# Performance work log

Measured on AMD Instinct MI355X. Metric: run time of the kernel, lower is better.

## Reference

```python
import jax, jax.numpy as jnp
import numpy as np

B, D, H, L = 131072, 128, 128, 4
LN_EPS = 1e-5


def _layernorm(x, gamma, beta):
    mu = jnp.mean(x, axis=-1, keepdims=True)
    var = jnp.mean(jnp.square(x - mu), axis=-1, keepdims=True)
    return (x - mu) * jax.lax.rsqrt(var + LN_EPS) * gamma + beta


def setup_inputs() -> dict:
    key = jax.random.key(0)
    ks = jax.random.split(key, 12)
    t = jax.random.uniform(ks[0], (1,), dtype=jnp.float32)
    p = jax.random.normal(ks[1], (B, D), dtype=jnp.float32)
    w = jax.random.normal(ks[2], (B, D), dtype=jnp.float32)
    # VectorField parameters (torch default inits approximated with scaled normals)
    W_in = jax.random.normal(ks[3], (H, D), dtype=jnp.float32) * (1.0 / np.sqrt(D))
    b_in = jax.random.normal(ks[4], (H,), dtype=jnp.float32) * 0.01
    # FourierFeature buffers, scale=1.0 (hard-coded in VectorField)
    fw = jax.random.normal(ks[5], (L, H), dtype=jnp.float32) * 1.0
    fb = jax.random.uniform(ks[6], (L, H), dtype=jnp.float32) * 1.0
    gamma = jnp.ones((L, H), dtype=jnp.float32)
    beta = jnp.zeros((L, H), dtype=jnp.float32)
    Wl = jax.random.normal(ks[7], (L, H, H), dtype=jnp.float32) * (1.0 / np.sqrt(H))
    bl = jax.random.normal(ks[8], (L, H), dtype=jnp.float32) * 0.01
    W_out = jax.random.normal(ks[9], (D, H), dtype=jnp.float32) * (1.0 / np.sqrt(H))
    b_out = jax.random.normal(ks[10], (D,), dtype=jnp.float32) * 0.01
    return {"t": t, "p": p, "w": w, "W_in": W_in, "b_in": b_in, "fw": fw,
            "fb": fb, "gamma": gamma, "beta": beta, "Wl": Wl, "bl": bl,
            "W_out": W_out, "b_out": b_out}


def reference(t, p, w, W_in, b_in, fw, fb, gamma, beta, Wl, bl, W_out, b_out):
    # VectorField.forward: all ops act per-row, so batched vjp == vmapped per-sample vjp
    def vf(pp):  # pp: [B, D]
        h = pp @ W_in.T + b_in                      # [B, H]
        for i in range(L):
            h = h + jnp.sin(t * fw[i] + fb[i])      # time embedding, broadcast [H]
            h = jax.nn.softplus(h)
            h = _layernorm(h, gamma[i], beta[i])
            h = h @ Wl[i].T + bl[i]
        return h @ W_out.T + b_out                  # [B, D]

    dp, vjp_fn = jax.vjp(vf, p)
    dw = -vjp_fn(w)[0]
    return dp, dw
```

## Files before the change

kernel.cpp:

```cpp
#include <hip/hip_runtime.h>

typedef unsigned short u16;
typedef unsigned int   u32;
typedef __attribute__((ext_vector_type(8))) short bf16x8;
typedef __attribute__((ext_vector_type(4))) float f32x4;

#define NB 131072
#define LN_EPS 1e-5f
#define EX_STRIDE 136

__device__ __forceinline__ u16 f2b(float f){
  union { __bf16 h; u16 u; } c; c.h = (__bf16)f; return c.u;
}
__device__ __forceinline__ float upk(u32 pr, int hi){
  union { u32 u; float f; } c; c.u = hi ? (pr & 0xFFFF0000u) : (pr << 16); return c.f;
}
__device__ __forceinline__ float rowsum16(float x){
  x += __shfl_xor(x, 1);
  x += __shfl_xor(x, 2);
  x += __shfl_xor(x, 4);
  x += __shfl_xor(x, 8);
  return x;
}
__device__ __forceinline__ bf16x8 cvt8(const float* __restrict__ s){
  f32x4 x0 = *(const f32x4*)s;
  f32x4 x1 = *(const f32x4*)(s + 4);
  bf16x8 r;
  r[0]=(short)f2b(x0[0]); r[1]=(short)f2b(x0[1]);
  r[2]=(short)f2b(x0[2]); r[3]=(short)f2b(x0[3]);
  r[4]=(short)f2b(x1[0]); r[5]=(short)f2b(x1[1]);
  r[6]=(short)f2b(x1[2]); r[7]=(short)f2b(x1[3]);
  return r;
}

__device__ __forceinline__ void glds16(const u16* g, u16* l){
  __builtin_amdgcn_global_load_lds(
      (const __attribute__((address_space(1))) void*)g,
      (__attribute__((address_space(3))) void*)l, 16, 0, 0);
}
__device__ __forceinline__ void stageB(const u16* __restrict__ packB, int m,
                                       u16* __restrict__ bst, int wave, int lane){
  const u16* src = packB + m*16384 + wave*512 + lane*8;
  u16*       dst = bst   + wave*512;
  #pragma unroll
  for (int k = 0; k < 8; k++)
    glds16(src + k*2048, dst + k*2048);
}

__device__ __forceinline__ void gemm16(const bf16x8 a[4], const u16* __restrict__ Blds,
                                       int lane, f32x4 C[8]){
  const bf16x8* Bf = (const bf16x8*)Blds;
  #pragma unroll
  for (int nt = 0; nt < 8; nt++){
    f32x4 c = {0.f, 0.f, 0.f, 0.f};
    #pragma unroll
    for (int kt = 0; kt < 4; kt++){
      bf16x8 b = Bf[(nt*4 + kt)*64 + lane];
      c = __builtin_amdgcn_mfma_f32_16x16x32_bf16(a[kt], b, c, 0, 0, 0);
    }
    C[nt] = c;
  }
}

__global__ void prep_kernel(const float* __restrict__ t,   const float* __restrict__ W_in,
                            const float* __restrict__ b_in,const float* __restrict__ fw,
                            const float* __restrict__ fb,  const float* __restrict__ gamma,
                            const float* __restrict__ beta,const float* __restrict__ Wl,
                            const float* __restrict__ bl,  const float* __restrict__ W_out,
                            const float* __restrict__ b_out,
                            u16* __restrict__ packB, float* __restrict__ vecs)
{
  int bid = blockIdx.x, tid = threadIdx.x;
  if (bid < 768){
    int e    = bid*256 + tid;
    int m    = e >> 14;
    int r    = e & 16383;
    int fi   = r >> 9;
    int lane = (r >> 3) & 63;
    int j    = r & 7;
    int nt = fi >> 2, kt = fi & 3;
    int k = kt*32 + (lane >> 4)*8 + j;
    int n = nt*16 + (lane & 15);
    const float* src; bool tr;
    if      (m == 0){ src = W_in;              tr = true;  }
    else if (m <= 4){ src = Wl + (m-1)*16384;  tr = true;  }
    else if (m == 5){ src = W_out;             tr = true;  }
    else if (m == 6){ src = W_out;             tr = false; }
    else if (m <=10){ src = Wl + (m-7)*16384;  tr = false; }
    else            { src = W_in;              tr = false; }
    float v = tr ? src[n*128 + k] : src[k*128 + n];
    if      (m >= 1 && m <= 4)  v *= gamma[(m-1)*128 + k];
    else if (m >= 7 && m <= 10) v *= gamma[(m-7)*128 + n];
    packB[e] = f2b(v);
  } else if (bid < 770){
    int idx = (bid - 768)*256 + tid;
    vecs[idx] = sinf(t[0] * fw[idx] + fb[idx]);
  } else if (bid < 772){
    int gid = (bid - 770)*256 + tid;
    int i = gid >> 7, o = gid & 127;
    const float* Wr = Wl + i*16384 + o*128;
    const float* be = beta + i*128;
    float acc = bl[gid];
    for (int k2 = 0; k2 < 128; k2++) acc += be[k2] * Wr[k2];
    vecs[512 + gid] = acc;
  } else {
    if (tid < 128) vecs[1024 + tid]        = b_in[tid];
    else           vecs[1152 + (tid-128)]  = b_out[tid-128];
  }
}

__global__ __launch_bounds__(256, 2)
void fused_vf(const float* __restrict__ p, const float* __restrict__ w,
              const u16* __restrict__ packB, const float* __restrict__ vecs,
              float* __restrict__ dp_out, float* __restrict__ dw_out)
{
  __shared__ __align__(16) u16  exch[4 * 16 * EX_STRIDE];
  __shared__ __align__(16) u16  bstage[16384];
  __shared__ float sv[1024];

  const int tid  = threadIdx.x;
  const int wave = tid >> 6, lane = tid & 63;
  const int l15  = lane & 15, quad = lane >> 4;
  u16* ex = exch + wave * 16 * EX_STRIDE;

  stageB(packB, 0, bstage, wave, lane);
  for (int idx = tid; idx < 1024; idx += 256) sv[idx] = vecs[idx];
  const float* sS   = sv;
  const float* sBl  = sv + 512;
  const float* gBin  = vecs + 1024;
  const float* gBout = vecs + 1152;

  const long rowBase = (long)blockIdx.x * 64 + wave * 16;

  u32   sp_ck[4][8][2];
  float mus[4][4];
  float invs[4][4];

  bf16x8 a[4];
  f32x4  C[8];

  {
    const float* pr = p + (size_t)(rowBase + l15)*128 + quad*8;
    #pragma unroll
    for (int kt = 0; kt < 4; kt++) a[kt] = cvt8(pr + kt*32);
  }
  __syncthreads();
  gemm16(a, bstage, lane, C);
  #pragma unroll
  for (int nt = 0; nt < 8; nt++){
    float bv = gBin[nt*16 + l15];
    #pragma unroll
    for (int r = 0; r < 4; r++) C[nt][r] += bv;
  }

  #pragma unroll
  for (int i = 0; i < 4; i++){
    __syncthreads();
    stageB(packB, 1+i, bstage, wave, lane);
    float sum[4] = {0,0,0,0}, ssq[4] = {0,0,0,0};
    #pragma unroll
    for (int nt = 0; nt < 8; nt++){
      float se = sS[i*128 + nt*16 + l15];
      #pragma unroll
      for (int r = 0; r < 4; r++){
        float x  = C[nt][r] + se;
        float e  = __expf(-fabsf(x));
        float li = __logf(1.0f + e);
        float sp = fmaxf(x, 0.0f) + li;
        u16 sb = f2b(sp);
        if (r & 1) sp_ck[i][nt][r>>1] |= ((u32)sb) << 16; else sp_ck[i][nt][r>>1] = sb;
        sum[r] += sp; ssq[r] += sp*sp;
        C[nt][r] = sp;
      }
    }
    float mu[4], inv[4];
    #pragma unroll
    for (int r = 0; r < 4; r++){
      float m1 = rowsum16(sum[r]) * (1.0f/128.0f);
      float m2 = rowsum16(ssq[r]) * (1.0f/128.0f);
      float var = m2 - m1*m1;
      mu[r] = m1; inv[r] = rsqrtf(fmaxf(var, 0.0f) + LN_EPS);
      mus[i][r] = m1; invs[i][r] = inv[r];
    }
    #pragma unroll
    for (int nt = 0; nt < 8; nt++)
      #pragma unroll
      for (int r = 0; r < 4; r++){
        float xh = (C[nt][r] - mu[r]) * inv[r];
        ex[(quad*4 + r)*EX_STRIDE + nt*16 + l15] = f2b(xh);
      }
    __syncthreads();
    {
      const u16* rp = ex + l15*EX_STRIDE + quad*8;
      #pragma unroll
      for (int kt = 0; kt < 4; kt++) a[kt] = *(const bf16x8*)(rp + kt*32);
    }
    gemm16(a, bstage, lane, C);
    #pragma unroll
    for (int nt = 0; nt < 8; nt++){
      float bv = sBl[i*128 + nt*16 + l15];
      #pragma unroll
      for (int r = 0; r < 4; r++) C[nt][r] += bv;
    }
  }

  __syncthreads();
  stageB(packB, 5, bstage, wave, lane);
  #pragma unroll
  for (int nt = 0; nt < 8; nt++)
    #pragma unroll
    for (int r = 0; r < 4; r++)
      ex[(quad*4 + r)*EX_STRIDE + nt*16 + l15] = f2b(C[nt][r]);
  __syncthreads();
  {
    const u16* rp = ex + l15*EX_STRIDE + quad*8;
    #pragma unroll
    for (int kt = 0; kt < 4; kt++) a[kt] = *(const bf16x8*)(rp + kt*32);
  }
  gemm16(a, bstage, lane, C);
  {
    float* gp = dp_out + (size_t)rowBase*128;
    #pragma unroll
    for (int nt = 0; nt < 8; nt++){
      float bv = gBout[nt*16 + l15];
      #pragma unroll
      for (int r = 0; r < 4; r++)
        gp[(size_t)(quad*4 + r)*128 + nt*16 + l15] = C[nt][r] + bv;
    }
  }

  __syncthreads();
  stageB(packB, 6, bstage, wave, lane);
  {
    const float* wr = w + (size_t)(rowBase + l15)*128 + quad*8;
    #pragma unroll
    for (int kt = 0; kt < 4; kt++) a[kt] = cvt8(wr + kt*32);
  }
  __syncthreads();
  gemm16(a, bstage, lane, C);
  __syncthreads();
  stageB(packB, 10, bstage, wave, lane);

  #pragma unroll
  for (int ii = 0; ii < 4; ii++){
    const int i = 3 - ii;
    #pragma unroll
    for (int nt = 0; nt < 8; nt++)
      #pragma unroll
      for (int r = 0; r < 4; r++)
        ex[(quad*4 + r)*EX_STRIDE + nt*16 + l15] = f2b(C[nt][r]);
    __syncthreads();
    {
      const u16* rp = ex + l15*EX_STRIDE + quad*8;
      #pragma unroll
      for (int kt = 0; kt < 4; kt++) a[kt] = *(const bf16x8*)(rp + kt*32);
    }
    gemm16(a, bstage, lane, C);
    __syncthreads();
    stageB(packB, (ii < 3) ? (7 + (2 - ii)) : 11, bstage, wave, lane);
    float s1[4] = {0,0,0,0}, s2[4] = {0,0,0,0};
    #pragma unroll
    for (int nt = 0; nt < 8; nt++)
      #pragma unroll
      for (int r = 0; r < 4; r++){
        float sp = upk(sp_ck[i][nt][r>>1], r & 1);
        float xh = (sp - mus[i][r]) * invs[i][r];
        float gx = C[nt][r];
        s1[r] += gx; s2[r] += gx * xh;
        C[nt][r] = gx;
      }
    float m1[4], m2[4];
    #pragma unroll
    for (int r = 0; r < 4; r++){
      m1[r] = rowsum16(s1[r]) * (1.0f/128.0f);
      m2[r] = rowsum16(s2[r]) * (1.0f/128.0f);
    }
    #pragma unroll
    for (int nt = 0; nt < 8; nt++)
      #pragma unroll
      for (int r = 0; r < 4; r++){
        float sp = upk(sp_ck[i][nt][r>>1], r & 1);
        float xh = (sp - mus[i][r]) * invs[i][r];
        float sg = 1.0f - __expf(-sp);
        float gu = invs[i][r] * (C[nt][r] - m1[r] - xh * m2[r]);
        C[nt][r] = gu * sg;
      }
  }

  #pragma unroll
  for (int nt = 0; nt < 8; nt++)
    #pragma unroll
    for (int r = 0; r < 4; r++)
      ex[(quad*4 + r)*EX_STRIDE + nt*16 + l15] = f2b(C[nt][r]);
  __syncthreads();
  {
    const u16* rp = ex + l15*EX_STRIDE + quad*8;
    #pragma unroll
    for (int kt = 0; kt < 4; kt++) a[kt] = *(const bf16x8*)(rp + kt*32);
  }
  gemm16(a, bstage, lane, C);
  {
    float* gp = dw_out + (size_t)rowBase*128;
    #pragma unroll
    for (int nt = 0; nt < 8; nt++)
      #pragma unroll
      for (int r = 0; r < 4; r++)
        gp[(size_t)(quad*4 + r)*128 + nt*16 + l15] = -C[nt][r];
  }
}

extern "C" void kernel_launch(void* const* d_in, const int* in_sizes, int n_in,
                              void* d_out, int out_size, void* d_ws, size_t ws_size,
                              hipStream_t stream)
{
  const float* t     = (const float*)d_in[0];
  const float* p     = (const float*)d_in[1];
  const float* w     = (const float*)d_in[2];
  const float* W_in  = (const float*)d_in[3];
  const float* b_in  = (const float*)d_in[4];
  const float* fw    = (const float*)d_in[5];
  const float* fb    = (const float*)d_in[6];
  const float* gamma = (const float*)d_in[7];
  const float* beta  = (const float*)d_in[8];
  const float* Wl    = (const float*)d_in[9];
  const float* bl    = (const float*)d_in[10];
  const float* W_out = (const float*)d_in[11];
  const float* b_out = (const float*)d_in[12];

  u16*   packB = (u16*)d_ws;
  float* vecs  = (float*)((char*)d_ws + 12*16384*2);

  prep_kernel<<<773, 256, 0, stream>>>(t, W_in, b_in, fw, fb, gamma, beta,
                                       Wl, bl, W_out, b_out, packB, vecs);

  float* dp = (float*)d_out;
  float* dw = (float*)d_out + (size_t)NB * 128;
  fused_vf<<<NB/64, 256, 0, stream>>>(p, w, packB, vecs, dp, dw);
}
```

Baseline: 386.0 us.

## Swap MFMA operands so each lane holds one row's features

The MFMA operands are swapped so weights are the A operand and activations the B operand, which transposes the accumulator layout: each lane now holds four consecutive features of a single row. Row reductions for LayerNorm shrink from four 4-step shuffle trees per row set to one 2-step shuffle across quads. LDS exchange writes become packed 8-byte stores, and the global output stores and bias loads become 16-byte vector accesses. This relies on the packed weight layout being valid under the swapped operand roles. It also reduces the per-lane mean and inverse-std state, which may lower register pressure.

After: 356.3 us. 7.7% less time.

```diff
diff --git a/kernel.cpp b/kernel.cpp
--- a/kernel.cpp
+++ b/kernel.cpp
@@ -4,6 +4,7 @@
 typedef unsigned int   u32;
 typedef __attribute__((ext_vector_type(8))) short bf16x8;
 typedef __attribute__((ext_vector_type(4))) float f32x4;
+typedef __attribute__((ext_vector_type(2))) unsigned int u32x2;
 
 #define NB 131072
 #define LN_EPS 1e-5f
@@ -12,14 +13,15 @@
 __device__ __forceinline__ u16 f2b(float f){
   union { __bf16 h; u16 u; } c; c.h = (__bf16)f; return c.u;
 }
+__device__ __forceinline__ u32 pk2(float a, float b){
+  return (u32)f2b(a) | ((u32)f2b(b) << 16);
+}
 __device__ __forceinline__ float upk(u32 pr, int hi){
   union { u32 u; float f; } c; c.u = hi ? (pr & 0xFFFF0000u) : (pr << 16); return c.f;
 }
-__device__ __forceinline__ float rowsum16(float x){
-  x += __shfl_xor(x, 1);
-  x += __shfl_xor(x, 2);
-  x += __shfl_xor(x, 4);
-  x += __shfl_xor(x, 8);
+__device__ __forceinline__ float qsum(float x){
+  x += __shfl_xor(x, 16);
+  x += __shfl_xor(x, 32);
   return x;
 }
 __device__ __forceinline__ bf16x8 cvt8(const float* __restrict__ s){
@@ -47,18 +49,18 @@
     glds16(src + k*2048, dst + k*2048);
 }
 
-__device__ __forceinline__ void gemm16(const bf16x8 a[4], const u16* __restrict__ Blds,
-                                       int lane, f32x4 C[8]){
-  const bf16x8* Bf = (const bf16x8*)Blds;
-  #pragma unroll
-  for (int nt = 0; nt < 8; nt++){
+__device__ __forceinline__ void gemm16s(const bf16x8 x[4], const u16* __restrict__ Blds,
+                                        int lane, f32x4 C[8]){
+  const bf16x8* Wf = (const bf16x8*)Blds;
+  #pragma unroll
+  for (int mt = 0; mt < 8; mt++){
     f32x4 c = {0.f, 0.f, 0.f, 0.f};
     #pragma unroll
     for (int kt = 0; kt < 4; kt++){
-      bf16x8 b = Bf[(nt*4 + kt)*64 + lane];
-      c = __builtin_amdgcn_mfma_f32_16x16x32_bf16(a[kt], b, c, 0, 0, 0);
-    }
-    C[nt] = c;
+      bf16x8 wfrag = Wf[(mt*4 + kt)*64 + lane];
+      c = __builtin_amdgcn_mfma_f32_16x16x32_bf16(wfrag, x[kt], c, 0, 0, 0);
+    }
+    C[mt] = c;
   }
 }
 
@@ -116,116 +118,100 @@
 {
   __shared__ __align__(16) u16  exch[4 * 16 * EX_STRIDE];
   __shared__ __align__(16) u16  bstage[16384];
-  __shared__ float sv[1024];
+  __shared__ __align__(16) float sv[1024];
 
   const int tid  = threadIdx.x;
   const int wave = tid >> 6, lane = tid & 63;
   const int l15  = lane & 15, quad = lane >> 4;
   u16* ex = exch + wave * 16 * EX_STRIDE;
+  u16*       exw = ex + l15*EX_STRIDE + quad*4;
+  const u16* exr = ex + l15*EX_STRIDE + quad*8;
 
   stageB(packB, 0, bstage, wave, lane);
   for (int idx = tid; idx < 1024; idx += 256) sv[idx] = vecs[idx];
-  const float* sS   = sv;
-  const float* sBl  = sv + 512;
+  const float* sS    = sv;
+  const float* sBl   = sv + 512;
   const float* gBin  = vecs + 1024;
   const float* gBout = vecs + 1152;
 
   const long rowBase = (long)blockIdx.x * 64 + wave * 16;
 
   u32   sp_ck[4][8][2];
-  float mus[4][4];
-  float invs[4][4];
-
-  bf16x8 a[4];
+  float mus[4];
+  float invs[4];
+
+  bf16x8 x[4];
   f32x4  C[8];
 
   {
     const float* pr = p + (size_t)(rowBase + l15)*128 + quad*8;
     #pragma unroll
-    for (int kt = 0; kt < 4; kt++) a[kt] = cvt8(pr + kt*32);
-  }
-  __syncthreads();
-  gemm16(a, bstage, lane, C);
-  #pragma unroll
-  for (int nt = 0; nt < 8; nt++){
-    float bv = gBin[nt*16 + l15];
-    #pragma unroll
-    for (int r = 0; r < 4; r++) C[nt][r] += bv;
-  }
+    for (int kt = 0; kt < 4; kt++) x[kt] = cvt8(pr + kt*32);
+  }
+  __syncthreads();
+  gemm16s(x, bstage, lane, C);
+  #pragma unroll
+  for (int mt = 0; mt < 8; mt++)
+    C[mt] += *(const f32x4*)(gBin + mt*16 + quad*4);
 
   #pragma unroll
   for (int i = 0; i < 4; i++){
     __syncthreads();
     stageB(packB, 1+i, bstage, wave, lane);
-    float sum[4] = {0,0,0,0}, ssq[4] = {0,0,0,0};
-    #pragma unroll
-    for (int nt = 0; nt < 8; nt++){
-      float se = sS[i*128 + nt*16 + l15];
+    float sum = 0.f, ssq = 0.f;
+    #pragma unroll
+    for (int mt = 0; mt < 8; mt++){
+      f32x4 se = *(const f32x4*)(sS + i*128 + mt*16 + quad*4);
       #pragma unroll
       for (int r = 0; r < 4; r++){
-        float x  = C[nt][r] + se;
-        float e  = __expf(-fabsf(x));
-        float li = __logf(1.0f + e);
-        float sp = fmaxf(x, 0.0f) + li;
+        float a_ = C[mt][r] + se[r];
+        float e  = __expf(-fabsf(a_));
+        float sp = fmaxf(a_, 0.0f) + __logf(1.0f + e);
         u16 sb = f2b(sp);
-        if (r & 1) sp_ck[i][nt][r>>1] |= ((u32)sb) << 16; else sp_ck[i][nt][r>>1] = sb;
-        sum[r] += sp; ssq[r] += sp*sp;
-        C[nt][r] = sp;
+        if (r & 1) sp_ck[i][mt][r>>1] |= ((u32)sb) << 16; else sp_ck[i][mt][r>>1] = sb;
+        sum += sp; ssq += sp*sp;
+        C[mt][r] = sp;
       }
     }
-    float mu[4], inv[4];
-    #pragma unroll
-    for (int r = 0; r < 4; r++){
-      float m1 = rowsum16(sum[r]) * (1.0f/128.0f);
-      float m2 = rowsum16(ssq[r]) * (1.0f/128.0f);
-      float var = m2 - m1*m1;
-      mu[r] = m1; inv[r] = rsqrtf(fmaxf(var, 0.0f) + LN_EPS);
-      mus[i][r] = m1; invs[i][r] = inv[r];
-    }
-    #pragma unroll
-    for (int nt = 0; nt < 8; nt++)
-      #pragma unroll
-      for (int r = 0; r < 4; r++){
-        float xh = (C[nt][r] - mu[r]) * inv[r];
-        ex[(quad*4 + r)*EX_STRIDE + nt*16 + l15] = f2b(xh);
-      }
+    float m1 = qsum(sum) * (1.0f/128.0f);
+    float m2 = qsum(ssq) * (1.0f/128.0f);
+    float inv = rsqrtf(fmaxf(m2 - m1*m1, 0.0f) + LN_EPS);
+    mus[i] = m1; invs[i] = inv;
+    #pragma unroll
+    for (int mt = 0; mt < 8; mt++){
+      u32x2 v;
+      v[0] = pk2((C[mt][0]-m1)*inv, (C[mt][1]-m1)*inv);
+      v[1] = pk2((C[mt][2]-m1)*inv, (C[mt][3]-m1)*inv);
+      *(u32x2*)(exw + mt*16) = v;
+    }
     __syncthreads();
-    {
-      const u16* rp = ex + l15*EX_STRIDE + quad*8;
-      #pragma unroll
-      for (int kt = 0; kt < 4; kt++) a[kt] = *(const bf16x8*)(rp + kt*32);
-    }
-    gemm16(a, bstage, lane, C);
-    #pragma unroll
-    for (int nt = 0; nt < 8; nt++){
-      float bv = sBl[i*128 + nt*16 + l15];
-      #pragma unroll
-      for (int r = 0; r < 4; r++) C[nt][r] += bv;
-    }
+    #pragma unroll
+    for (int kt = 0; kt < 4; kt++) x[kt] = *(const bf16x8*)(exr + kt*32);
+    gemm16s(x, bstage, lane, C);
+    #pragma unroll
+    for (int mt = 0; mt < 8; mt++)
+      C[mt] += *(const f32x4*)(sBl + i*128 + mt*16 + quad*4);
   }
 
   __syncthreads();
   stageB(packB, 5, bstage, wave, lane);
   #pragma unroll
-  for (int nt = 0; nt < 8; nt++)
-    #pragma unroll
-    for (int r = 0; r < 4; r++)
-      ex[(quad*4 + r)*EX_STRIDE + nt*16 + l15] = f2b(C[nt][r]);
-  __syncthreads();
+  for (int mt = 0; mt < 8; mt++){
+    u32x2 v;
+    v[0] = pk2(C[mt][0], C[mt][1]);
+    v[1] = pk2(C[mt][2], C[mt][3]);
+    *(u32x2*)(exw + mt*16) = v;
+  }
+  __syncthreads();
+  #pragma unroll
+  for (int kt = 0; kt < 4; kt++) x[kt] = *(const bf16x8*)(exr + kt*32);
+  gemm16s(x, bstage, lane, C);
   {
-    const u16* rp = ex + l15*EX_STRIDE + quad*8;
-    #pragma unroll
-    for (int kt = 0; kt < 4; kt++) a[kt] = *(const bf16x8*)(rp + kt*32);
-  }
-  gemm16(a, bstage, lane, C);
-  {
-    float* gp = dp_out + (size_t)rowBase*128;
-    #pragma unroll
-    for (int nt = 0; nt < 8; nt++){
-      float bv = gBout[nt*16 + l15];
-      #pragma unroll
-      for (int r = 0; r < 4; r++)
-        gp[(size_t)(quad*4 + r)*128 + nt*16 + l15] = C[nt][r] + bv;
+    float* gp = dp_out + (size_t)(rowBase + l15)*128;
+    #pragma unroll
+    for (int mt = 0; mt < 8; mt++){
+      f32x4 o = C[mt] + *(const f32x4*)(gBout + mt*16 + quad*4);
+      *(f32x4*)(gp + mt*16 + quad*4) = o;
     }
   }
 
@@ -234,10 +220,10 @@
   {
     const float* wr = w + (size_t)(rowBase + l15)*128 + quad*8;
     #pragma unroll
-    for (int kt = 0; kt < 4; kt++) a[kt] = cvt8(wr + kt*32);
-  }
-  __syncthreads();
-  gemm16(a, bstage, lane, C);
+    for (int kt = 0; kt < 4; kt++) x[kt] = cvt8(wr + kt*32);
+  }
+  __syncthreads();
+  gemm16s(x, bstage, lane, C);
   __syncthreads();
   stageB(packB, 10, bstage, wave, lane);
 
@@ -245,67 +231,60 @@
   for (int ii = 0; ii < 4; ii++){
     const int i = 3 - ii;
     #pragma unroll
-    for (int nt = 0; nt < 8; nt++)
-      #pragma unroll
-      for (int r = 0; r < 4; r++)
-        ex[(quad*4 + r)*EX_STRIDE + nt*16 + l15] = f2b(C[nt][r]);
+    for (int mt = 0; mt < 8; mt++){
+      u32x2 v;
+      v[0] = pk2(C[mt][0], C[mt][1]);
+      v[1] = pk2(C[mt][2], C[mt][3]);
+      *(u32x2*)(exw + mt*16) = v;
+    }
     __syncthreads();
-    {
-      const u16* rp = ex + l15*EX_STRIDE + quad*8;
-      #pragma unroll
-      for (int kt = 0; kt < 4; kt++) a[kt] = *(const bf16x8*)(rp + kt*32);
-    }
-    gemm16(a, bstage, lane, C);
+    #pragma unroll
+    for (int kt = 0; kt < 4; kt++) x[kt] = *(const bf16x8*)(exr + kt*32);
+    gemm16s(x, bstage, lane, C);
     __syncthreads();
     stageB(packB, (ii < 3) ? (7 + (2 - ii)) : 11, bstage, wave, lane);
-    float s1[4] = {0,0,0,0}, s2[4] = {0,0,0,0};
-    #pragma unroll
-    for (int nt = 0; nt < 8; nt++)
+    float s1 = 0.f, s2 = 0.f;
+    #pragma unroll
+    for (int mt = 0; mt < 8; mt++)
       #pragma unroll
       for (int r = 0; r < 4; r++){
-        float sp = upk(sp_ck[i][nt][r>>1], r & 1);
-        float xh = (sp - mus[i][r]) * invs[i][r];
-        float gx = C[nt][r];
-        s1[r] += gx; s2[r] += gx * xh;
-        C[nt][r] = gx;
+        float sp = upk(sp_ck[i][mt][r>>1], r & 1);
+        float xh = (sp - mus[i]) * invs[i];
+        float gx = C[mt][r];
+        s1 += gx; s2 += gx * xh;
       }
-    float m1[4], m2[4];
-    #pragma unroll
-    for (int r = 0; r < 4; r++){
-      m1[r] = rowsum16(s1[r]) * (1.0f/128.0f);
-      m2[r] = rowsum16(s2[r]) * (1.0f/128.0f);
-    }
-    #pragma unroll
-    for (int nt = 0; nt < 8; nt++)
+    float m1 = qsum(s1) * (1.0f/128.0f);
+    float m2 = qsum(s2) * (1.0f/128.0f);
+    #pragma unroll
+    for (int mt = 0; mt < 8; mt++)
       #pragma unroll
       for (int r = 0; r < 4; r++){
-        float sp = upk(sp_ck[i][nt][r>>1], r & 1);
-        float xh = (sp - mus[i][r]) * invs[i][r];
+        float sp = upk(sp_ck[i][mt][r>>1], r & 1);
+        float xh = (sp - mus[i]) * invs[i];
         float sg = 1.0f - __expf(-sp);
-        float gu = invs[i][r] * (C[nt][r] - m1[r] - xh * m2[r]);
-        C[nt][r] = gu * sg;
+        float gu = invs[i] * (C[mt][r] - m1 - xh * m2);
+        C[mt][r] = gu * sg;
       }
   }
 
   #pragma unroll
-  for (int nt = 0; nt < 8; nt++)
-    #pragma unroll
-    for (int r = 0; r < 4; r++)
-      ex[(quad*4 + r)*EX_STRIDE + nt*16 + l15] = f2b(C[nt][r]);
-  __syncthreads();
+  for (int mt = 0; mt < 8; mt++){
+    u32x2 v;
+    v[0] = pk2(C[mt][0], C[mt][1]);
+    v[1] = pk2(C[mt][2], C[mt][3]);
+    *(u32x2*)(exw + mt*16) = v;
+  }
+  __syncthreads();
+  #pragma unroll
+  for (int kt = 0; kt < 4; kt++) x[kt] = *(const bf16x8*)(exr + kt*32);
+  gemm16s(x, bstage, lane, C);
   {
-    const u16* rp = ex + l15*EX_STRIDE + quad*8;
-    #pragma unroll
-    for (int kt = 0; kt < 4; kt++) a[kt] = *(const bf16x8*)(rp + kt*32);
-  }
-  gemm16(a, bstage, lane, C);
-  {
-    float* gp = dw_out + (size_t)rowBase*128;
-    #pragma unroll
-    for (int nt = 0; nt < 8; nt++)
-      #pragma unroll
-      for (int r = 0; r < 4; r++)
-        gp[(size_t)(quad*4 + r)*128 + nt*16 + l15] = -C[nt][r];
+    float* gp = dw_out + (size_t)(rowBase + l15)*128;
+    #pragma unroll
+    for (int mt = 0; mt < 8; mt++){
+      f32x4 o = -C[mt];
+      *(f32x4*)(gp + mt*16 + quad*4) = o;
+    }
   }
 }
 
```
